# Optimization experiments

Hardware: AMD Instinct MI355X
Metric: run time of the kernel (lower is better)

Reference implementation:

```python
import jax, jax.numpy as jnp
import numpy as np

G, N, E, F, C, H = 2, 20000, 160000, 128, 64, 8
NEG_SLOPE = 0.2


def setup_inputs() -> dict:
    key = jax.random.key(0)
    ks = jax.random.split(key, 16)
    def w(k, shape, fan_in):
        return jax.random.normal(k, shape, jnp.float32) * (1.0 / np.sqrt(fan_in))
    z = lambda *s: jnp.zeros(s, jnp.float32)
    return {
        "x": jax.random.normal(ks[0], (G, N, F), jnp.float32),
        "edge_index": jax.random.randint(ks[1], (G, 2, E), 0, N, jnp.int32),
        "edge_weight": jax.random.uniform(ks[2], (G, E), jnp.float32),
        "Wl1": w(ks[3], (F, H * C), F), "bl1": z(H * C),
        "Wr1": w(ks[4], (F, H * C), F), "br1": z(H * C),
        "We1": w(ks[5], (1, H * C), 1),
        "att1": w(ks[6], (H, C), C),
        "bias1": z(H * C),
        "Wl2": w(ks[7], (H * C, C), H * C), "bl2": z(C),
        "Wr2": w(ks[8], (H * C, C), H * C), "br2": z(C),
        "We2": w(ks[9], (1, C), 1),
        "att2": w(ks[10], (1, C), C),
        "bias2": z(C),
        "Wg": w(ks[11], (C, C), C), "bg": z(C),
        "Wn": w(ks[12], (2 * C, C), 2 * C), "bn": z(C),
        "Wo": w(ks[13], (C, 1), C), "bo": z(1),
    }


def _segment_softmax(logits, seg, n):
    m = jax.ops.segment_max(logits, seg, num_segments=n)
    ex = jnp.exp(logits - m[seg])
    den = jax.ops.segment_sum(ex, seg, num_segments=n)
    return ex / den[seg]


def _gatv2(x, src, dst, eattr, Wl, bl, Wr, br, We, att, bias, heads, concat):
    # Faithful PyG GATv2Conv (share_weights=False, edge_dim=1).
    n = x.shape[0]
    hc = Wl.shape[1]
    c = hc // heads
    xl = (x @ Wl + bl).reshape(n, heads, c)   # lin_l (source / message)
    xr = (x @ Wr + br).reshape(n, heads, c)   # lin_r (target)
    ee = (eattr @ We).reshape(-1, heads, c)   # lin_edge (bias=False)
    s = jax.nn.leaky_relu(xl[src] + xr[dst] + ee, NEG_SLOPE)  # [Etot, H, C]
    logit = jnp.einsum('ehc,hc->eh', s, att)
    alpha = _segment_softmax(logit, dst, n)   # softmax over incoming edges
    out = jax.ops.segment_sum(alpha[..., None] * xl[src], dst, num_segments=n)
    out = out.reshape(n, hc) if concat else out.mean(axis=1)
    return out + bias


def _forward(edge_index, x, edge_weight, Wl1, bl1, Wr1, br1, We1, att1, bias1,
             Wl2, bl2, Wr2, br2, We2, att2, bias2, Wg, bg, Wn, bn, Wo, bo):
    n = x.shape[1]
    def per_graph(xg, eig, ewg):
        src, dst = eig[0], eig[1]
        ea = ewg[:, None]  # edge_weight.unsqueeze(-1), edge_dim=1
        # add_self_loops with fill_value='mean' (mean of edge_attr grouped by dst)
        cnt = jax.ops.segment_sum(jnp.ones_like(ewg), dst, num_segments=n)
        loop = jax.ops.segment_sum(ea, dst, num_segments=n) / jnp.clip(cnt, 1.0)[:, None]
        ar = jnp.arange(n, dtype=src.dtype)
        src2 = jnp.concatenate([src, ar])
        dst2 = jnp.concatenate([dst, ar])
        ea2 = jnp.concatenate([ea, loop], axis=0)
        h = jax.nn.elu(_gatv2(xg, src2, dst2, ea2, Wl1, bl1, Wr1, br1, We1, att1, bias1, H, True))
        h = jax.nn.elu(_gatv2(h, src2, dst2, ea2, Wl2, bl2, Wr2, br2, We2, att2, bias2, 1, False))
        return h
    h = jax.vmap(per_graph)(x, edge_index, edge_weight)      # [G, N, C]
    g_emb = h.max(axis=1)                                    # global_max_pool per graph
    Gv = g_emb.max(axis=0)                                   # max over graphs -> [C]
    Gv = jax.nn.relu(Gv @ Wg + bg)
    Hc = jnp.concatenate([h, jnp.broadcast_to(Gv, h.shape)], axis=-1)  # [G,N,2C]
    h2 = jax.nn.relu(Hc @ Wn + bn)
    return (h2 @ Wo + bo)[..., 0]                            # [G, N] logits


def reference(x, edge_index, edge_weight, Wl1, bl1, Wr1, br1, We1, att1, bias1,
              Wl2, bl2, Wr2, br2, We2, att2, bias2, Wg, bg, Wn, bn, Wo, bo):
    return _forward(edge_index, x, edge_weight, Wl1, bl1, Wr1, br1, We1, att1, bias1,
                    Wl2, bl2, Wr2, br2, We2, att2, bias2, Wg, bg, Wn, bn, Wo, bo)
```

## Files before the change

### kernel.cpp

```cpp
#include <hip/hip_runtime.h>
#include <hip/hip_bf16.h>
#include <cstdint>
#include <cstddef>

#define NEG_SLOPE 0.2f

static constexpr int Gg = 2;
static constexpr int Nn = 20000;
static constexpr int Ee = 160000;
static constexpr int Ff = 128;
static constexpr int Cc = 64;
static constexpr int HC = 512;
static constexpr int GN = Gg * Nn;
static constexpr int GNP = 40064;
static constexpr int DEGMAX = 48;

typedef __attribute__((ext_vector_type(8))) short short8;
typedef __attribute__((ext_vector_type(4))) float floatx4;

__device__ __forceinline__ float bf2f(unsigned short b) {
    return __uint_as_float(((unsigned)b) << 16);
}
__device__ __forceinline__ unsigned short f2bf(float x) {
    unsigned u = __float_as_uint(x);
    unsigned r = 0x7fffu + ((u >> 16) & 1u);
    return (unsigned short)((u + r) >> 16);
}
__device__ __forceinline__ void unpack8(const uint4 p, float* f) {
    f[0] = __uint_as_float(p.x << 16); f[1] = __uint_as_float(p.x & 0xffff0000u);
    f[2] = __uint_as_float(p.y << 16); f[3] = __uint_as_float(p.y & 0xffff0000u);
    f[4] = __uint_as_float(p.z << 16); f[5] = __uint_as_float(p.z & 0xffff0000u);
    f[6] = __uint_as_float(p.w << 16); f[7] = __uint_as_float(p.w & 0xffff0000u);
}
__device__ __forceinline__ void unpack4(const uint2 p, float* f) {
    f[0] = __uint_as_float(p.x << 16); f[1] = __uint_as_float(p.x & 0xffff0000u);
    f[2] = __uint_as_float(p.y << 16); f[3] = __uint_as_float(p.y & 0xffff0000u);
}
__device__ __forceinline__ unsigned encf(float x) {
    unsigned u = __float_as_uint(x);
    return (u & 0x80000000u) ? ~u : (u | 0x80000000u);
}
__device__ __forceinline__ float decf(unsigned e) {
    return __uint_as_float((e & 0x80000000u) ? (e ^ 0x80000000u) : ~e);
}

__global__ void castprep_k(const float* __restrict__ x, unsigned short* __restrict__ xb,
                           const float* __restrict__ Wl1, const float* __restrict__ Wr1,
                           const float* __restrict__ bl1, const float* __restrict__ br1,
                           const float* __restrict__ Wl2, const float* __restrict__ Wr2,
                           const float* __restrict__ bl2, const float* __restrict__ br2,
                           unsigned short* __restrict__ Wt1, unsigned short* __restrict__ Wt2,
                           float* __restrict__ b1cat, float* __restrict__ b2cat,
                           int* __restrict__ cnt, unsigned* __restrict__ gmax) {
    int t = blockIdx.x * 256 + threadIdx.x;
    size_t base = (size_t)t * 4;
    if (base < (size_t)GNP * Ff) {
        ushort4 ov;
        if (base < (size_t)GN * Ff) {
            float4 v = *(const float4*)(x + base);
            ov.x = f2bf(v.x); ov.y = f2bf(v.y); ov.z = f2bf(v.z); ov.w = f2bf(v.w);
        } else {
            ov.x = ov.y = ov.z = ov.w = 0;
        }
        *(ushort4*)(xb + base) = ov;
    }
    if (t < 1024 * 128) {
        int n = t >> 7, k = t & 127;
        float v = (n < 512) ? Wl1[(size_t)k * 512 + n] : Wr1[(size_t)k * 512 + n - 512];
        Wt1[t] = f2bf(v);
    }
    if (t < 128 * 512) {
        int n = t >> 9, k = t & 511;
        float v = (n < 64) ? Wl2[(size_t)k * 64 + n] : Wr2[(size_t)k * 64 + n - 64];
        Wt2[t] = f2bf(v);
    }
    if (t < 1024) b1cat[t] = (t < 512) ? bl1[t] : br1[t - 512];
    if (t < 128)  b2cat[t] = (t < 64) ? bl2[t] : br2[t - 64];
    if (t < GN)   cnt[t] = 0;
    if (t < 1024) gmax[t] = 0u;
}

__global__ void build_csr_k(const int* __restrict__ ei, const float* __restrict__ ew,
                            int* __restrict__ cnt, int2* __restrict__ sedge) {
    int idx = blockIdx.x * 256 + threadIdx.x;
    if (idx >= Gg * Ee) return;
    int g = (idx >= Ee) ? 1 : 0;
    int e = idx - g * Ee;
    int src = ei[(size_t)g * 2 * Ee + e];
    int dst = ei[(size_t)g * 2 * Ee + Ee + e];
    float wv = ew[idx];
    int node = g * Nn + dst;
    int pos = atomicAdd(&cnt[node], 1);
    if (pos < DEGMAX) {
        int2 v; v.x = src; v.y = __float_as_int(wv);
        sedge[(size_t)node * DEGMAX + pos] = v;
    }
}

template <int K>
__global__ __launch_bounds__(256) void mfma_gemm_k(const unsigned short* __restrict__ A, int lda,
                                                   const unsigned short* __restrict__ Bt,
                                                   const float* __restrict__ bias,
                                                   unsigned short* __restrict__ Cg, int ldc,
                                                   int Mreal) {
    __shared__ unsigned short As[128 * 32];
    __shared__ unsigned short Bs[128 * 32];
    const int t = threadIdx.x;
    const int lane = t & 63;
    const int wid = t >> 6;
    const int wm = wid >> 1, wn = wid & 1;
    const int m0 = blockIdx.x * 128;
    const int n0 = blockIdx.y * 128;

    floatx4 acc[4][4] = {};

    const int jrow = t >> 2;
    const int js = t & 3;
    const int wavebase = (t & 192) * 16;

    for (int k0 = 0; k0 < K; k0 += 32) {
#pragma unroll
        for (int r = 0; r < 2; ++r) {
            int row = jrow + r * 64;
            int c = js ^ ((row >> 1) & 3);
            const unsigned short* gA = A + (size_t)(m0 + row) * lda + k0 + c * 8;
            const unsigned short* gB = Bt + (size_t)(n0 + row) * K + k0 + c * 8;
            __builtin_amdgcn_global_load_lds(
                (const __attribute__((address_space(1))) void*)gA,
                (__attribute__((address_space(3))) void*)((char*)As + r * 4096 + wavebase),
                16, 0, 0);
            __builtin_amdgcn_global_load_lds(
                (const __attribute__((address_space(1))) void*)gB,
                (__attribute__((address_space(3))) void*)((char*)Bs + r * 4096 + wavebase),
                16, 0, 0);
        }
        __syncthreads();

        const int lrow = lane & 15, lc = lane >> 4;
        short8 af[4], bf[4];
#pragma unroll
        for (int i2 = 0; i2 < 4; ++i2) {
            int rA = wm * 64 + i2 * 16 + lrow;
            int sA = lc ^ ((rA >> 1) & 3);
            af[i2] = *(const short8*)((const char*)As + (rA * 4 + sA) * 16);
        }
#pragma unroll
        for (int j2 = 0; j2 < 4; ++j2) {
            int rB = wn * 64 + j2 * 16 + lrow;
            int sB = lc ^ ((rB >> 1) & 3);
            bf[j2] = *(const short8*)((const char*)Bs + (rB * 4 + sB) * 16);
        }
#pragma unroll
        for (int i2 = 0; i2 < 4; ++i2)
#pragma unroll
            for (int j2 = 0; j2 < 4; ++j2)
                acc[i2][j2] = __builtin_amdgcn_mfma_f32_16x16x32_bf16(bf[j2], af[i2], acc[i2][j2], 0, 0, 0);
        __syncthreads();
    }

    const int mrow = m0 + wm * 64 + (lane & 15);
    const int ncol0 = n0 + wn * 64 + ((lane >> 4) << 2);
    float4 bq[4];
#pragma unroll
    for (int j2 = 0; j2 < 4; ++j2) bq[j2] = *(const float4*)(bias + ncol0 + j2 * 16);
#pragma unroll
    for (int i2 = 0; i2 < 4; ++i2) {
        int m = mrow + i2 * 16;
        if (m < Mreal) {
#pragma unroll
            for (int j2 = 0; j2 < 4; ++j2) {
                ushort4 ov;
                ov.x = f2bf(acc[i2][j2][0] + bq[j2].x);
                ov.y = f2bf(acc[i2][j2][1] + bq[j2].y);
                ov.z = f2bf(acc[i2][j2][2] + bq[j2].z);
                ov.w = f2bf(acc[i2][j2][3] + bq[j2].w);
                *(ushort4*)(Cg + (size_t)m * ldc + ncol0 + j2 * 16) = ov;
            }
        }
    }
}

__global__ __launch_bounds__(256) void agg1_k(const unsigned short* xlr,
                                              const int2* __restrict__ sedge,
                                              const int* __restrict__ cnt,
                                              const float* __restrict__ att1, const float* __restrict__ We1,
                                              const float* __restrict__ bias1,
                                              unsigned short* h1, float* __restrict__ loopw) {
    const int tid = threadIdx.x;
    const int lane = tid & 63;
    const int half = (tid >> 6) & 1;
    const int slot = tid >> 7;
    const int node = (blockIdx.x << 1) + slot;
    const int g = (node >= Nn) ? 1 : 0;

    float attv[8], wev[8];
    {
        float4 a0 = *(const float4*)(att1 + lane * 8);
        float4 a1 = *(const float4*)(att1 + lane * 8 + 4);
        attv[0] = a0.x; attv[1] = a0.y; attv[2] = a0.z; attv[3] = a0.w;
        attv[4] = a1.x; attv[5] = a1.y; attv[6] = a1.z; attv[7] = a1.w;
        float4 w0 = *(const float4*)(We1 + lane * 8);
        float4 w1 = *(const float4*)(We1 + lane * 8 + 4);
        wev[0] = w0.x; wev[1] = w0.y; wev[2] = w0.z; wev[3] = w0.w;
        wev[4] = w1.x; wev[5] = w1.y; wev[6] = w1.z; wev[7] = w1.w;
    }
    float xrv[8];
    unpack8(((const uint4*)(xlr + (size_t)node * 1024 + 512))[lane], xrv);

    const int ec = cnt[node];
    const int mid = ec >> 1;
    const int lo = half ? mid : 0;
    const int hi = half ? ec : mid;
    const int2* ep = sedge + (size_t)node * DEGMAX;
    const uint4* rowb = (const uint4*)(xlr + (size_t)g * Nn * 1024) + lane;

    float lsum = 0.f, wsum = 0.f;
    float acc[8] = {};

    int e = lo;
    uint4 r0, r1; int2 s0v, s1v;
    if (e < hi)     { s0v = ep[e];     r0 = rowb[(size_t)s0v.x * 128]; }
    if (e + 1 < hi) { s1v = ep[e + 1]; r1 = rowb[(size_t)s1v.x * 128]; }
    while (e + 1 < hi) {
        uint4 r2, r3; int2 s2v, s3v;
        if (e + 2 < hi) { s2v = ep[e + 2]; r2 = rowb[(size_t)s2v.x * 128]; }
        if (e + 3 < hi) { s3v = ep[e + 3]; r3 = rowb[(size_t)s3v.x * 128]; }
        float xa[8], xb_[8];
        unpack8(r0, xa);
        unpack8(r1, xb_);
        float wa = __int_as_float(s0v.y), wb = __int_as_float(s1v.y);
        wsum += wa + wb;
        float ta = 0.f, tb = 0.f;
#pragma unroll
        for (int j = 0; j < 8; ++j) {
            float sa = xa[j] + fmaf(wa, wev[j], xrv[j]);
            float sb = xb_[j] + fmaf(wb, wev[j], xrv[j]);
            sa = fmaxf(sa, NEG_SLOPE * sa);
            sb = fmaxf(sb, NEG_SLOPE * sb);
            ta = fmaf(sa, attv[j], ta);
            tb = fmaf(sb, attv[j], tb);
        }
        ta += __shfl_xor(ta, 1); tb += __shfl_xor(tb, 1);
        ta += __shfl_xor(ta, 2); tb += __shfl_xor(tb, 2);
        ta += __shfl_xor(ta, 4); tb += __shfl_xor(tb, 4);
        float pa = __expf(ta), pb = __expf(tb);
        lsum += pa + pb;
#pragma unroll
        for (int j = 0; j < 8; ++j) acc[j] = fmaf(pa, xa[j], fmaf(pb, xb_[j], acc[j]));
        r0 = r2; s0v = s2v; r1 = r3; s1v = s3v;
        e += 2;
    }
    if (e < hi) {
        float xa[8];
        unpack8(r0, xa);
        float wa = __int_as_float(s0v.y);
        wsum += wa;
        float ta = 0.f;
#pragma unroll
        for (int j = 0; j < 8; ++j) {
            float sa = xa[j] + fmaf(wa, wev[j], xrv[j]);
            sa = fmaxf(sa, NEG_SLOPE * sa);
            ta = fmaf(sa, attv[j], ta);
        }
        ta += __shfl_xor(ta, 1); ta += __shfl_xor(ta, 2); ta += __shfl_xor(ta, 4);
        float pa = __expf(ta);
        lsum += pa;
#pragma unroll
        for (int j = 0; j < 8; ++j) acc[j] = fmaf(pa, xa[j], acc[j]);
    }

    __shared__ float sacc[2][64][9];
    __shared__ float sls[2][64];
    __shared__ float sws[2][64];
    if (half == 1) {
#pragma unroll
        for (int j = 0; j < 8; ++j) sacc[slot][lane][j] = acc[j];
        sls[slot][lane] = lsum;
        sws[slot][lane] = wsum;
    }
    __syncthreads();
    if (half == 0) {
#pragma unroll
        for (int j = 0; j < 8; ++j) acc[j] += sacc[slot][lane][j];
        lsum += sls[slot][lane];
        wsum += sws[slot][lane];
        float lw = wsum / fmaxf((float)ec, 1.f);

        float xv[8];
        unpack8(((const uint4*)(xlr + (size_t)node * 1024))[lane], xv);
        float tp = 0.f;
#pragma unroll
        for (int j = 0; j < 8; ++j) {
            float s = xv[j] + fmaf(lw, wev[j], xrv[j]);
            s = fmaxf(s, NEG_SLOPE * s);
            tp = fmaf(s, attv[j], tp);
        }
        tp += __shfl_xor(tp, 1); tp += __shfl_xor(tp, 2); tp += __shfl_xor(tp, 4);
        float p = __expf(tp);
        lsum += p;
#pragma unroll
        for (int j = 0; j < 8; ++j) acc[j] = fmaf(p, xv[j], acc[j]);

        float inv = 1.f / lsum;
        float4 b0 = *(const float4*)(bias1 + lane * 8);
        float4 b1 = *(const float4*)(bias1 + lane * 8 + 4);
        float bvv[8] = {b0.x, b0.y, b0.z, b0.w, b1.x, b1.y, b1.z, b1.w};
        float ov[8];
#pragma unroll
        for (int j = 0; j < 8; ++j) {
            float o = fmaf(acc[j], inv, bvv[j]);
            ov[j] = o > 0.f ? o : (__expf(o) - 1.f);
        }
        uint4 pk;
        pk.x = (unsigned)f2bf(ov[0]) | ((unsigned)f2bf(ov[1]) << 16);
        pk.y = (unsigned)f2bf(ov[2]) | ((unsigned)f2bf(ov[3]) << 16);
        pk.z = (unsigned)f2bf(ov[4]) | ((unsigned)f2bf(ov[5]) << 16);
        pk.w = (unsigned)f2bf(ov[6]) | ((unsigned)f2bf(ov[7]) << 16);
        ((uint4*)(h1 + (size_t)node * 1024))[lane] = pk;
        if (lane == 0) loopw[node] = lw;
    }
}

__global__ __launch_bounds__(256) void agg2_k(const unsigned short* __restrict__ xlr2,
                                              const int2* __restrict__ sedge,
                                              const int* __restrict__ cnt,
                                              const float* __restrict__ loopw,
                                              const float* __restrict__ att2, const float* __restrict__ We2,
                                              const float* __restrict__ bias2,
                                              float* __restrict__ hout, unsigned* __restrict__ gmax) {
    const int tid = threadIdx.x;
    const int lane = tid & 63;
    const int cs = lane & 15;
    const int sub = lane >> 4;
    const int w4 = (blockIdx.x << 2) + (tid >> 6);
    const int node = w4 * 4 + sub;
    const int g = (node >= Nn) ? 1 : 0;

    float4 av = *(const float4*)(att2 + cs * 4);
    float4 wv4 = *(const float4*)(We2 + cs * 4);
    float attv[4] = {av.x, av.y, av.z, av.w};
    float wevv[4] = {wv4.x, wv4.y, wv4.z, wv4.w};
    float xrv[4];
    unpack4(*(const uint2*)(xlr2 + (size_t)node * 128 + 64 + cs * 4), xrv);
    const unsigned short* rowb = xlr2 + (size_t)g * Nn * 128;

    float lsum, acc[4];
    {
        float lw = loopw[node];
        float xv[4];
        unpack4(*(const uint2*)(xlr2 + (size_t)node * 128 + cs * 4), xv);
        float tp = 0.f;
#pragma unroll
        for (int j = 0; j < 4; ++j) {
            float s = xv[j] + fmaf(lw, wevv[j], xrv[j]);
            s = fmaxf(s, NEG_SLOPE * s);
            tp = fmaf(s, attv[j], tp);
        }
        tp += __shfl_xor(tp, 1); tp += __shfl_xor(tp, 2);
        tp += __shfl_xor(tp, 4); tp += __shfl_xor(tp, 8);
        float p = __expf(tp);
        lsum = p;
#pragma unroll
        for (int j = 0; j < 4; ++j) acc[j] = p * xv[j];
    }

    const int ec = cnt[node];
    const int2* ep = sedge + (size_t)node * DEGMAX;

    uint2 r0 = {0, 0}, r1 = {0, 0};
    int2 s0v = {0, 0}, s1v = {0, 0};
    if (0 < ec) { s0v = ep[0]; r0 = *(const uint2*)(rowb + (size_t)s0v.x * 128 + cs * 4); }
    if (1 < ec) { s1v = ep[1]; r1 = *(const uint2*)(rowb + (size_t)s1v.x * 128 + cs * 4); }
    int e = 0;
    while (__any(e < ec)) {
        uint2 r2 = {0, 0}, r3 = {0, 0};
        int2 s2v = {0, 0}, s3v = {0, 0};
        if (e + 2 < ec) { s2v = ep[e + 2]; r2 = *(const uint2*)(rowb + (size_t)s2v.x * 128 + cs * 4); }
        if (e + 3 < ec) { s3v = ep[e + 3]; r3 = *(const uint2*)(rowb + (size_t)s3v.x * 128 + cs * 4); }
        bool v0 = (e < ec), v1 = (e + 1 < ec);
        float xa[4], xb_[4];
        unpack4(r0, xa);
        unpack4(r1, xb_);
        float wa = __int_as_float(s0v.y), wb = __int_as_float(s1v.y);
        float ta = 0.f, tb = 0.f;
#pragma unroll
        for (int j = 0; j < 4; ++j) {
            float sa = xa[j] + fmaf(wa, wevv[j], xrv[j]);
            float sb = xb_[j] + fmaf(wb, wevv[j], xrv[j]);
            sa = fmaxf(sa, NEG_SLOPE * sa);
            sb = fmaxf(sb, NEG_SLOPE * sb);
            ta = fmaf(sa, attv[j], ta);
            tb = fmaf(sb, attv[j], tb);
        }
        ta += __shfl_xor(ta, 1); tb += __shfl_xor(tb, 1);
        ta += __shfl_xor(ta, 2); tb += __shfl_xor(tb, 2);
        ta += __shfl_xor(ta, 4); tb += __shfl_xor(tb, 4);
        ta += __shfl_xor(ta, 8); tb += __shfl_xor(tb, 8);
        float pa = v0 ? __expf(ta) : 0.f;
        float pb = v1 ? __expf(tb) : 0.f;
        lsum += pa + pb;
#pragma unroll
        for (int j = 0; j < 4; ++j) acc[j] = fmaf(pa, xa[j], fmaf(pb, xb_[j], acc[j]));
        r0 = r2; s0v = s2v; r1 = r3; s1v = s3v;
        e += 2;
    }

    float inv = 1.f / lsum;
    float4 bv = *(const float4*)(bias2 + cs * 4);
    float bvv[4] = {bv.x, bv.y, bv.z, bv.w};
    float ov[4];
#pragma unroll
    for (int j = 0; j < 4; ++j) {
        float o = fmaf(acc[j], inv, bvv[j]);
        ov[j] = o > 0.f ? o : (__expf(o) - 1.f);
    }
    float4 o4;
    o4.x = ov[0]; o4.y = ov[1]; o4.z = ov[2]; o4.w = ov[3];
    *(float4*)(hout + (size_t)node * Cc + cs * 4) = o4;

    float mj[4];
#pragma unroll
    for (int j = 0; j < 4; ++j) {
        float m = ov[j];
        m = fmaxf(m, __shfl_xor(m, 16));
        m = fmaxf(m, __shfl_xor(m, 32));
        mj[j] = m;
    }
    __shared__ unsigned bm[64];
    if (tid < 64) bm[tid] = 0u;
    __syncthreads();
    if (sub == 0) {
#pragma unroll
        for (int j = 0; j < 4; ++j) atomicMax(&bm[cs * 4 + j], encf(mj[j]));
    }
    __syncthreads();
    if (tid < 64) atomicMax(&gmax[tid * 16], bm[tid]);
}

__global__ __launch_bounds__(256) void final_k(const float* __restrict__ h,
                                               const unsigned* __restrict__ gmax,
                                               const float* __restrict__ Wg, const float* __restrict__ bg,
                                               const float* __restrict__ Wn, const float* __restrict__ bn,
                                               const float* __restrict__ Wo, const float* __restrict__ bo,
                                               float* __restrict__ out) {
    __shared__ float wns[64 * 64];
    __shared__ float g0s[64], g1s[64], cvs[64];
    const int tid = threadIdx.x;
    for (int k = tid; k < 64 * 64; k += 256) wns[k] = Wn[k];
    if (tid < 64) g0s[tid] = decf(gmax[tid * 16]);
    __syncthreads();
    if (tid < 64) {
        float a = bg[tid];
        for (int c = 0; c < 64; ++c) a += g0s[c] * Wg[c * 64 + tid];
        g1s[tid] = fmaxf(a, 0.f);
    }
    __syncthreads();
    if (tid < 64) {
        float b = bn[tid];
        for (int c = 0; c < 64; ++c) b += g1s[c] * Wn[(64 + c) * 64 + tid];
        cvs[tid] = b;
    }
    __syncthreads();

    const int lane = tid & 63;
    const int cs = lane & 15;
    const int sub = lane >> 4;
    const int node = blockIdx.x * 16 + (tid >> 6) * 4 + sub;

    float4 h4 = *(const float4*)(h + (size_t)node * Cc + cs * 4);
    float hv[4] = {h4.x, h4.y, h4.z, h4.w};
    float inner[4] = {cvs[cs * 4 + 0], cvs[cs * 4 + 1], cvs[cs * 4 + 2], cvs[cs * 4 + 3]};
#pragma unroll
    for (int c = 0; c < 64; ++c) {
        float hc = __shfl(hv[c & 3], sub * 16 + (c >> 2));
        float4 wv = *(const float4*)&wns[c * 64 + cs * 4];
        inner[0] = fmaf(hc, wv.x, inner[0]);
        inner[1] = fmaf(hc, wv.y, inner[1]);
        inner[2] = fmaf(hc, wv.z, inner[2]);
        inner[3] = fmaf(hc, wv.w, inner[3]);
    }
    float4 wo4 = *(const float4*)(Wo + cs * 4);
    float woa[4] = {wo4.x, wo4.y, wo4.z, wo4.w};
    float t = 0.f;
#pragma unroll
    for (int j = 0; j < 4; ++j) {
        float v = fmaxf(inner[j], 0.f);
        t = fmaf(v, woa[j], t);
    }
    t += __shfl_xor(t, 1); t += __shfl_xor(t, 2);
    t += __shfl_xor(t, 4); t += __shfl_xor(t, 8);
    if (cs == 0) out[node] = t + bo[0];
}

extern "C" void kernel_launch(void* const* d_in, const int* in_sizes, int n_in,
                              void* d_out, int out_size, void* d_ws, size_t ws_size,
                              hipStream_t stream) {
    const float* x     = (const float*)d_in[0];
    const int*   ei    = (const int*)d_in[1];
    const float* ew    = (const float*)d_in[2];
    const float* Wl1   = (const float*)d_in[3];
    const float* bl1v  = (const float*)d_in[4];
    const float* Wr1   = (const float*)d_in[5];
    const float* br1v  = (const float*)d_in[6];
    const float* We1   = (const float*)d_in[7];
    const float* att1  = (const float*)d_in[8];
    const float* bias1 = (const float*)d_in[9];
    const float* Wl2   = (const float*)d_in[10];
    const float* bl2v  = (const float*)d_in[11];
    const float* Wr2   = (const float*)d_in[12];
    const float* br2v  = (const float*)d_in[13];
    const float* We2   = (const float*)d_in[14];
    const float* att2  = (const float*)d_in[15];
    const float* bias2 = (const float*)d_in[16];
    const float* Wg    = (const float*)d_in[17];
    const float* bgv   = (const float*)d_in[18];
    const float* Wn    = (const float*)d_in[19];
    const float* bnv   = (const float*)d_in[20];
    const float* Wo    = (const float*)d_in[21];
    const float* bov   = (const float*)d_in[22];
    float* out = (float*)d_out;

    char* w = (char*)d_ws;
    size_t o = 0;
    auto take = [&](size_t b) -> char* {
        char* p = w + o;
        o += (b + 255) & ~(size_t)255;
        return p;
    };
    unsigned short* xlr1 = (unsigned short*)take((size_t)GNP * 1024 * 2);
    unsigned short* xb   = (unsigned short*)take((size_t)GNP * Ff * 2);
    unsigned short* xlr2 = (unsigned short*)take((size_t)GNP * 128 * 2);
    unsigned short* Wt1  = (unsigned short*)take(1024 * 128 * 2);
    unsigned short* Wt2  = (unsigned short*)take(128 * 512 * 2);
    float* b1cat = (float*)take(1024 * 4);
    float* b2cat = (float*)take(128 * 4);
    int*    cnt   = (int*)take((size_t)GN * 4);
    float*  loopw = (float*)take((size_t)GN * 4);
    int2*   sedge = (int2*)take((size_t)GN * DEGMAX * 8);
    unsigned* gmax = (unsigned*)take(1024 * 4);
    unsigned short* h1 = xlr1 + 512;
    float* hbuf = (float*)xb;

    castprep_k<<<((GNP * Ff / 4) + 255) / 256, 256, 0, stream>>>(
        x, xb, Wl1, Wr1, bl1v, br1v, Wl2, Wr2, bl2v, br2v, Wt1, Wt2, b1cat, b2cat, cnt, gmax);

    build_csr_k<<<(Gg * Ee + 255) / 256, 256, 0, stream>>>(ei, ew, cnt, sedge);

    mfma_gemm_k<Ff><<<dim3(GNP / 128, 8), 256, 0, stream>>>(xb, Ff, Wt1, b1cat, xlr1, 1024, GN);

    agg1_k<<<GN / 2, 256, 0, stream>>>(xlr1, sedge, cnt, att1, We1, bias1, h1, loopw);

    mfma_gemm_k<HC><<<dim3(GNP / 128, 1), 256, 0, stream>>>(h1, 1024, Wt2, b2cat, xlr2, 128, GN);

    agg2_k<<<GN / 16, 256, 0, stream>>>(xlr2, sedge, cnt, loopw, att2, We2, bias2, hbuf, gmax);

    final_k<<<GN / 16, 256, 0, stream>>>(hbuf, gmax, Wg, bgv, Wn, bnv, Wo, bov, out);

    (void)in_sizes; (void)n_in; (void)out_size; (void)ws_size;
}
```

Baseline: 347.6 us.

## Fuse CSR build into first GEMM and use one wave per node in agg1

Folds the edge-bucketing (CSR build) work into the prologue of the first MFMA GEMM kernel, removing one kernel launch. The GEMM grid of 313x8 blocks of 256 threads covers all 320000 edges, so every edge is still placed. The layer-1 aggregation now gives each node a single wavefront instead of splitting its edges across two waves and merging them through shared memory with a barrier. This drops the LDS reduction and syncthreads, but each wave walks twice as many edges serially, which lengthens the per-node latency chain.

New measurement: 336.2 us. -3.3%, faster.

```diff
diff --git a/kernel.cpp b/kernel.cpp
--- a/kernel.cpp
+++ b/kernel.cpp
@@ -80,29 +80,34 @@
     if (t < 1024) gmax[t] = 0u;
 }
 
-__global__ void build_csr_k(const int* __restrict__ ei, const float* __restrict__ ew,
-                            int* __restrict__ cnt, int2* __restrict__ sedge) {
-    int idx = blockIdx.x * 256 + threadIdx.x;
-    if (idx >= Gg * Ee) return;
-    int g = (idx >= Ee) ? 1 : 0;
-    int e = idx - g * Ee;
-    int src = ei[(size_t)g * 2 * Ee + e];
-    int dst = ei[(size_t)g * 2 * Ee + Ee + e];
-    float wv = ew[idx];
-    int node = g * Nn + dst;
-    int pos = atomicAdd(&cnt[node], 1);
-    if (pos < DEGMAX) {
-        int2 v; v.x = src; v.y = __float_as_int(wv);
-        sedge[(size_t)node * DEGMAX + pos] = v;
-    }
-}
-
-template <int K>
+template <int K, bool EDGES>
 __global__ __launch_bounds__(256) void mfma_gemm_k(const unsigned short* __restrict__ A, int lda,
                                                    const unsigned short* __restrict__ Bt,
                                                    const float* __restrict__ bias,
                                                    unsigned short* __restrict__ Cg, int ldc,
-                                                   int Mreal) {
+                                                   int Mreal,
+                                                   const int* __restrict__ ei,
+                                                   const float* __restrict__ ew,
+                                                   int* __restrict__ cnt,
+                                                   int2* __restrict__ sedge) {
+    if (EDGES) {
+        int bid = blockIdx.y * gridDim.x + blockIdx.x;
+        int idx = bid * 256 + threadIdx.x;
+        if (idx < Gg * Ee) {
+            int g = (idx >= Ee) ? 1 : 0;
+            int e = idx - g * Ee;
+            int src = ei[(size_t)g * 2 * Ee + e];
+            int dst = ei[(size_t)g * 2 * Ee + Ee + e];
+            float wv = ew[idx];
+            int node = g * Nn + dst;
+            int pos = atomicAdd(&cnt[node], 1);
+            if (pos < DEGMAX) {
+                int2 v; v.x = src; v.y = __float_as_int(wv);
+                sedge[(size_t)node * DEGMAX + pos] = v;
+            }
+        }
+    }
+
     __shared__ unsigned short As[128 * 32];
     __shared__ unsigned short Bs[128 * 32];
     const int t = threadIdx.x;
@@ -186,11 +191,9 @@
                                               const float* __restrict__ att1, const float* __restrict__ We1,
                                               const float* __restrict__ bias1,
                                               unsigned short* h1, float* __restrict__ loopw) {
-    const int tid = threadIdx.x;
-    const int lane = tid & 63;
-    const int half = (tid >> 6) & 1;
-    const int slot = tid >> 7;
-    const int node = (blockIdx.x << 1) + slot;
+    const int lane = threadIdx.x & 63;
+    const int node = (blockIdx.x << 2) + (threadIdx.x >> 6);
+    if (node >= GN) return;
     const int g = (node >= Nn) ? 1 : 0;
 
     float attv[8], wev[8];
@@ -208,23 +211,20 @@
     unpack8(((const uint4*)(xlr + (size_t)node * 1024 + 512))[lane], xrv);
 
     const int ec = cnt[node];
-    const int mid = ec >> 1;
-    const int lo = half ? mid : 0;
-    const int hi = half ? ec : mid;
     const int2* ep = sedge + (size_t)node * DEGMAX;
     const uint4* rowb = (const uint4*)(xlr + (size_t)g * Nn * 1024) + lane;
 
     float lsum = 0.f, wsum = 0.f;
     float acc[8] = {};
 
-    int e = lo;
     uint4 r0, r1; int2 s0v, s1v;
-    if (e < hi)     { s0v = ep[e];     r0 = rowb[(size_t)s0v.x * 128]; }
-    if (e + 1 < hi) { s1v = ep[e + 1]; r1 = rowb[(size_t)s1v.x * 128]; }
-    while (e + 1 < hi) {
+    if (ec > 0) { s0v = ep[0]; r0 = rowb[(size_t)s0v.x * 128]; }
+    if (ec > 1) { s1v = ep[1]; r1 = rowb[(size_t)s1v.x * 128]; }
+    int e = 0;
+    while (e + 1 < ec) {
         uint4 r2, r3; int2 s2v, s3v;
-        if (e + 2 < hi) { s2v = ep[e + 2]; r2 = rowb[(size_t)s2v.x * 128]; }
-        if (e + 3 < hi) { s3v = ep[e + 3]; r3 = rowb[(size_t)s3v.x * 128]; }
+        if (e + 2 < ec) { s2v = ep[e + 2]; r2 = rowb[(size_t)s2v.x * 128]; }
+        if (e + 3 < ec) { s3v = ep[e + 3]; r3 = rowb[(size_t)s3v.x * 128]; }
         float xa[8], xb_[8];
         unpack8(r0, xa);
         unpack8(r1, xb_);
@@ -250,7 +250,7 @@
         r0 = r2; s0v = s2v; r1 = r3; s1v = s3v;
         e += 2;
     }
-    if (e < hi) {
+    if (e < ec) {
         float xa[8];
         unpack8(r0, xa);
         float wa = __int_as_float(s0v.y);
@@ -269,23 +269,8 @@
         for (int j = 0; j < 8; ++j) acc[j] = fmaf(pa, xa[j], acc[j]);
     }
 
-    __shared__ float sacc[2][64][9];
-    __shared__ float sls[2][64];
-    __shared__ float sws[2][64];
-    if (half == 1) {
-#pragma unroll
-        for (int j = 0; j < 8; ++j) sacc[slot][lane][j] = acc[j];
-        sls[slot][lane] = lsum;
-        sws[slot][lane] = wsum;
-    }
-    __syncthreads();
-    if (half == 0) {
-#pragma unroll
-        for (int j = 0; j < 8; ++j) acc[j] += sacc[slot][lane][j];
-        lsum += sls[slot][lane];
-        wsum += sws[slot][lane];
-        float lw = wsum / fmaxf((float)ec, 1.f);
-
+    float lw = wsum / fmaxf((float)ec, 1.f);
+    {
         float xv[8];
         unpack8(((const uint4*)(xlr + (size_t)node * 1024))[lane], xv);
         float tp = 0.f;
@@ -300,25 +285,25 @@
         lsum += p;
 #pragma unroll
         for (int j = 0; j < 8; ++j) acc[j] = fmaf(p, xv[j], acc[j]);
-
-        float inv = 1.f / lsum;
-        float4 b0 = *(const float4*)(bias1 + lane * 8);
-        float4 b1 = *(const float4*)(bias1 + lane * 8 + 4);
-        float bvv[8] = {b0.x, b0.y, b0.z, b0.w, b1.x, b1.y, b1.z, b1.w};
-        float ov[8];
-#pragma unroll
-        for (int j = 0; j < 8; ++j) {
-            float o = fmaf(acc[j], inv, bvv[j]);
-            ov[j] = o > 0.f ? o : (__expf(o) - 1.f);
-        }
-        uint4 pk;
-        pk.x = (unsigned)f2bf(ov[0]) | ((unsigned)f2bf(ov[1]) << 16);
-        pk.y = (unsigned)f2bf(ov[2]) | ((unsigned)f2bf(ov[3]) << 16);
-        pk.z = (unsigned)f2bf(ov[4]) | ((unsigned)f2bf(ov[5]) << 16);
-        pk.w = (unsigned)f2bf(ov[6]) | ((unsigned)f2bf(ov[7]) << 16);
-        ((uint4*)(h1 + (size_t)node * 1024))[lane] = pk;
-        if (lane == 0) loopw[node] = lw;
-    }
+    }
+
+    float inv = 1.f / lsum;
+    float4 b0 = *(const float4*)(bias1 + lane * 8);
+    float4 b1 = *(const float4*)(bias1 + lane * 8 + 4);
+    float bvv[8] = {b0.x, b0.y, b0.z, b0.w, b1.x, b1.y, b1.z, b1.w};
+    float ov[8];
+#pragma unroll
+    for (int j = 0; j < 8; ++j) {
+        float o = fmaf(acc[j], inv, bvv[j]);
+        ov[j] = o > 0.f ? o : (__expf(o) - 1.f);
+    }
+    uint4 pk;
+    pk.x = (unsigned)f2bf(ov[0]) | ((unsigned)f2bf(ov[1]) << 16);
+    pk.y = (unsigned)f2bf(ov[2]) | ((unsigned)f2bf(ov[3]) << 16);
+    pk.z = (unsigned)f2bf(ov[4]) | ((unsigned)f2bf(ov[5]) << 16);
+    pk.w = (unsigned)f2bf(ov[6]) | ((unsigned)f2bf(ov[7]) << 16);
+    ((uint4*)(h1 + (size_t)node * 1024))[lane] = pk;
+    if (lane == 0) loopw[node] = lw;
 }
 
 __global__ __launch_bounds__(256) void agg2_k(const unsigned short* __restrict__ xlr2,
@@ -544,13 +529,13 @@
     castprep_k<<<((GNP * Ff / 4) + 255) / 256, 256, 0, stream>>>(
         x, xb, Wl1, Wr1, bl1v, br1v, Wl2, Wr2, bl2v, br2v, Wt1, Wt2, b1cat, b2cat, cnt, gmax);
 
-    build_csr_k<<<(Gg * Ee + 255) / 256, 256, 0, stream>>>(ei, ew, cnt, sedge);
-
-    mfma_gemm_k<Ff><<<dim3(GNP / 128, 8), 256, 0, stream>>>(xb, Ff, Wt1, b1cat, xlr1, 1024, GN);
-
-    agg1_k<<<GN / 2, 256, 0, stream>>>(xlr1, sedge, cnt, att1, We1, bias1, h1, loopw);
-
-    mfma_gemm_k<HC><<<dim3(GNP / 128, 1), 256, 0, stream>>>(h1, 1024, Wt2, b2cat, xlr2, 128, GN);
+    mfma_gemm_k<Ff, true><<<dim3(GNP / 128, 8), 256, 0, stream>>>(
+        xb, Ff, Wt1, b1cat, xlr1, 1024, GN, ei, ew, cnt, sedge);
+
+    agg1_k<<<GN / 4, 256, 0, stream>>>(xlr1, sedge, cnt, att1, We1, bias1, h1, loopw);
+
+    mfma_gemm_k<HC, false><<<dim3(GNP / 128, 1), 256, 0, stream>>>(
+        h1, 1024, Wt2, b2cat, xlr2, 128, GN, nullptr, nullptr, nullptr, nullptr);
 
     agg2_k<<<GN / 16, 256, 0, stream>>>(xlr2, sedge, cnt, loopw, att2, We2, bias2, hbuf, gmax);
 
```
